# Optimization experiments

Measured on AMD Instinct MI355X. Metric: run time of the kernel, lower is better.

Reference implementation:

```python
import jax, jax.numpy as jnp
import numpy as np

D_MODEL = 1024
N = 32  # d_state // 2
L_LEN = 4096


def setup_inputs() -> dict:
    key = jax.random.key(0)
    k1, k2, k3 = jax.random.split(key, 3)
    dt_min, dt_max = 1e-3, 1e-1
    log_dt = jax.random.uniform(k1, (D_MODEL,), dtype=jnp.float32) * (
        np.log(dt_max) - np.log(dt_min)
    ) + np.log(dt_min)
    C_ri = jax.random.normal(k2, (D_MODEL, N, 2), dtype=jnp.float32)
    log_A_real = jnp.log(0.5 * jnp.ones((D_MODEL, N), dtype=jnp.float32))
    A_imag = np.pi * jnp.broadcast_to(
        jnp.arange(N, dtype=jnp.float32)[None, :], (D_MODEL, N)
    )
    return {
        "L": L_LEN,
        "log_dt": log_dt,
        "C_ri": C_ri,
        "log_A_real": log_A_real,
        "A_imag": A_imag,
    }


def reference(L, log_dt, C_ri, log_A_real, A_imag):
    dt = jnp.exp(log_dt)  # (H,)
    C = C_ri[..., 0] + 1j * C_ri[..., 1]  # (H, N) complex
    A = -jnp.exp(log_A_real) + 1j * A_imag  # (H, N)
    dtA = A * dt[:, None]  # (H, N)
    # Vandermonde: exp(dtA * l) for l in [0, L)
    l = jnp.arange(L, dtype=jnp.float32)
    V = jnp.exp(dtA[:, :, None] * l[None, None, :])  # (H, N, L) complex
    Ceff = C * (jnp.exp(dtA) - 1.0) / A  # (H, N)
    K = 2.0 * jnp.einsum("hn,hnl->hl", Ceff, V).real  # (H, L)
    return K
```

## Files before the change

kernel.cpp:

```cpp
#include <hip/hip_runtime.h>


#define HD   1024
#define NS   32
#define LL   4096
#define BLK  256
#define NJ   (LL / BLK)

typedef float v2 __attribute__((ext_vector_type(2)));

__global__ __launch_bounds__(BLK) void s4d_kernel(
    const float* __restrict__ log_dt,
    const float* __restrict__ C_ri,
    const float* __restrict__ log_A_real,
    const float* __restrict__ A_imag,
    float* __restrict__ K)
{
    const int h   = blockIdx.x;
    const int tid = threadIdx.x;

    __shared__ v2 s_wr[NS / 2], s_wi[NS / 2];
    __shared__ v2 s_q[NS / 2];
    __shared__ v2 s_c2r[NS / 2], s_c2i[NS / 2];
    __shared__ v2 s_al2[NS / 2];
    __shared__ double s_rb[NS];

    const double TWO_PI     = 6.283185307179586;
    const double INV_TWO_PI = 0.15915494309189535;
    const float  TWO_PI_F   = 6.2831853f;

    if (tid < NS) {
        const int   n   = tid;
        const int   sl  = ((n & 15) << 1) | (n >> 4);
        const float dt  = expf(log_dt[h]);
        const float ar  = -expf(log_A_real[h * NS + n]);
        const float ai  = A_imag[h * NS + n];
        const float a   = ar * dt;
        const double bd = (double)ai * (double)dt;
        const float b   = (float)bd;

        const float e = expf(a);
        float sb, cb;
        sincosf(b, &sb, &cb);
        const float er = fmaf(e, cb, -1.0f);
        const float ei = e * sb;

        const float den = fmaf(ar, ar, ai * ai);
        const float inv = 1.0f / den;
        const float fr  = fmaf(er, ar,  ei * ai) * inv;
        const float fi  = fmaf(ei, ar, -er * ai) * inv;

        const float Cr = C_ri[(h * NS + n) * 2 + 0];
        const float Ci = C_ri[(h * NS + n) * 2 + 1];
        ((float*)s_c2r)[sl] = 2.0f * fmaf(Cr, fr, -Ci * fi);
        ((float*)s_c2i)[sl] = 2.0f * fmaf(Cr, fi,  Ci * fr);

        double ph = bd * 256.0;
        ph -= floor(ph * INV_TWO_PI) * TWO_PI;
        float sw, cw;
        sincosf((float)ph, &sw, &cw);
        const float e256 = expf(a * 256.0f);
        ((float*)s_wr)[sl]  = e256 * cw;
        ((float*)s_wi)[sl]  = e256 * sw;
        ((float*)s_q)[sl]   = e256 * e256;
        ((float*)s_al2)[sl] = a * 1.4426950408889634f;
        s_rb[n] = bd * INV_TWO_PI;
    }
    __syncthreads();

    v2 acc[NJ];
#pragma unroll
    for (int j = 0; j < NJ; ++j) acc[j] = (v2)(0.0f);

    const float t = (float)tid;

    for (int np = 0; np < NS / 2; ++np) {
        const v2 al2 = s_al2[np];
        const v2 wr  = s_wr[np];
        const v2 wi  = s_wi[np];
        const v2 q   = s_q[np];
        const v2 c2r = s_c2r[np];
        const v2 c2i = s_c2i[np];

        v2 mag;
        mag.x = __builtin_amdgcn_exp2f(al2.x * t);
        mag.y = __builtin_amdgcn_exp2f(al2.y * t);

        double r0 = s_rb[np] * (double)tid;        r0 -= floor(r0);
        double r1 = s_rb[np + 16] * (double)tid;   r1 -= floor(r1);
        const float f0 = (float)r0 * TWO_PI_F;
        const float f1 = (float)r1 * TWO_PI_F;

        v2 zr, zi;
        zr.x = mag.x * __cosf(f0);
        zr.y = mag.y * __cosf(f1);
        zi.x = mag.x * __sinf(f0);
        zi.y = mag.y * __sinf(f1);

        v2 u0 = c2r * zr - c2i * zi;
        v2 zwr = zr * wr - zi * wi;
        v2 zwi = zr * wi + zi * wr;
        v2 u1 = c2r * zwr - c2i * zwi;
        const v2 p = wr + wr;

        acc[0] += u0;
        acc[1] += u1;
#pragma unroll
        for (int j = 2; j < NJ; ++j) {
            const v2 u = p * u1 - q * u0;
            acc[j] += u;
            u0 = u1;
            u1 = u;
        }
    }

    float* out = K + h * LL + tid;
#pragma unroll
    for (int j = 0; j < NJ; ++j) out[j * BLK] = acc[j].x + acc[j].y;
}

extern "C" void kernel_launch(void* const* d_in, const int* in_sizes, int n_in,
                              void* d_out, int out_size, void* d_ws, size_t ws_size,
                              hipStream_t stream) {
    const float* log_dt     = (const float*)d_in[1];
    const float* C_ri       = (const float*)d_in[2];
    const float* log_A_real = (const float*)d_in[3];
    const float* A_imag     = (const float*)d_in[4];
    float* K = (float*)d_out;

    s4d_kernel<<<dim3(HD), dim3(BLK), 0, stream>>>(log_dt, C_ri, log_A_real, A_imag, K);
}
```

Baseline: 79.46 us.

## Split each channel across two blocks and replace double-precision phase with float split

Each channel's length is now split across two blocks, doubling the grid and halving the per-thread recurrence length and accumulator count, with launch bounds requesting higher occupancy. The double-precision phase reduction is replaced by a hi/lo float split of the phase rate using hardware fract and the native sin/cos builtins that take revolutions. The second recurrence seed is computed with fewer multiplies by rotating u0 directly. This targets slow FP64 work and poor latency hiding, at the cost of duplicated per-channel setup and some phase accuracy risk.

After: 79.28 us. Within noise of the previous version (-0.2%).

```diff
diff --git a/kernel.cpp b/kernel.cpp
--- a/kernel.cpp
+++ b/kernel.cpp
@@ -5,29 +5,32 @@
 #define NS   32
 #define LL   4096
 #define BLK  256
-#define NJ   (LL / BLK)
+#define JBLK 2
+#define NJ   (LL / (BLK * JBLK))
+#define GRID (HD * JBLK)
 
 typedef float v2 __attribute__((ext_vector_type(2)));
 
-__global__ __launch_bounds__(BLK) void s4d_kernel(
+__global__ __launch_bounds__(BLK, 8) void s4d_kernel(
     const float* __restrict__ log_dt,
     const float* __restrict__ C_ri,
     const float* __restrict__ log_A_real,
     const float* __restrict__ A_imag,
     float* __restrict__ K)
 {
-    const int h   = blockIdx.x;
+    const int bid = blockIdx.x;
+    const int h   = bid >> 1;
+    const int jb  = bid & 1;
     const int tid = threadIdx.x;
 
     __shared__ v2 s_wr[NS / 2], s_wi[NS / 2];
     __shared__ v2 s_q[NS / 2];
     __shared__ v2 s_c2r[NS / 2], s_c2i[NS / 2];
     __shared__ v2 s_al2[NS / 2];
-    __shared__ double s_rb[NS];
+    __shared__ v2 s_rh[NS / 2], s_rl[NS / 2];
 
     const double TWO_PI     = 6.283185307179586;
     const double INV_TWO_PI = 0.15915494309189535;
-    const float  TWO_PI_F   = 6.2831853f;
 
     if (tid < NS) {
         const int   n   = tid;
@@ -64,7 +67,11 @@
         ((float*)s_wi)[sl]  = e256 * sw;
         ((float*)s_q)[sl]   = e256 * e256;
         ((float*)s_al2)[sl] = a * 1.4426950408889634f;
-        s_rb[n] = bd * INV_TWO_PI;
+
+        const double rbd = bd * INV_TWO_PI;
+        const double rhd = rint(rbd * 256.0) * 0.00390625;
+        ((float*)s_rh)[sl] = (float)rhd;
+        ((float*)s_rl)[sl] = (float)(rbd - rhd);
     }
     __syncthreads();
 
@@ -72,8 +79,9 @@
 #pragma unroll
     for (int j = 0; j < NJ; ++j) acc[j] = (v2)(0.0f);
 
-    const float t = (float)tid;
+    const float t = (float)(tid + (jb << 11));
 
+#pragma unroll 1
     for (int np = 0; np < NS / 2; ++np) {
         const v2 al2 = s_al2[np];
         const v2 wr  = s_wr[np];
@@ -81,26 +89,24 @@
         const v2 q   = s_q[np];
         const v2 c2r = s_c2r[np];
         const v2 c2i = s_c2i[np];
+        const v2 rh  = s_rh[np];
+        const v2 rl  = s_rl[np];
 
-        v2 mag;
+        v2 mag, ph;
         mag.x = __builtin_amdgcn_exp2f(al2.x * t);
         mag.y = __builtin_amdgcn_exp2f(al2.y * t);
-
-        double r0 = s_rb[np] * (double)tid;        r0 -= floor(r0);
-        double r1 = s_rb[np + 16] * (double)tid;   r1 -= floor(r1);
-        const float f0 = (float)r0 * TWO_PI_F;
-        const float f1 = (float)r1 * TWO_PI_F;
+        ph.x  = __builtin_amdgcn_fractf(fmaf(rl.x, t, __builtin_amdgcn_fractf(rh.x * t)));
+        ph.y  = __builtin_amdgcn_fractf(fmaf(rl.y, t, __builtin_amdgcn_fractf(rh.y * t)));
 
         v2 zr, zi;
-        zr.x = mag.x * __cosf(f0);
-        zr.y = mag.y * __cosf(f1);
-        zi.x = mag.x * __sinf(f0);
-        zi.y = mag.y * __sinf(f1);
+        zr.x = mag.x * __builtin_amdgcn_cosf(ph.x);
+        zr.y = mag.y * __builtin_amdgcn_cosf(ph.y);
+        zi.x = mag.x * __builtin_amdgcn_sinf(ph.x);
+        zi.y = mag.y * __builtin_amdgcn_sinf(ph.y);
 
         v2 u0 = c2r * zr - c2i * zi;
-        v2 zwr = zr * wr - zi * wi;
-        v2 zwi = zr * wi + zi * wr;
-        v2 u1 = c2r * zwr - c2i * zwi;
+        v2 vv = c2r * zi + c2i * zr;
+        v2 u1 = wr * u0 - wi * vv;
         const v2 p = wr + wr;
 
         acc[0] += u0;
@@ -114,7 +120,7 @@
         }
     }
 
-    float* out = K + h * LL + tid;
+    float* out = K + h * LL + (jb << 11) + tid;
 #pragma unroll
     for (int j = 0; j < NJ; ++j) out[j * BLK] = acc[j].x + acc[j].y;
 }
@@ -128,5 +134,5 @@
     const float* A_imag     = (const float*)d_in[4];
     float* K = (float*)d_out;
 
-    s4d_kernel<<<dim3(HD), dim3(BLK), 0, stream>>>(log_dt, C_ri, log_A_real, A_imag, K);
+    s4d_kernel<<<dim3(GRID), dim3(BLK), 0, stream>>>(log_dt, C_ri, log_A_real, A_imag, K);
 }
```
